# Kernel optimization log

Hardware: AMD Instinct MI355X
Metric: run time of the kernel (lower is better)

The kernel has to match this reference:

```python
import jax, jax.numpy as jnp
import numpy as np

H = 128  # hidden size
I = 256  # input size

def setup_inputs() -> dict:
    key = jax.random.key(0)
    ks = jax.random.split(key, 12)
    s_ih = 1.0 / np.sqrt(H)
    inp = {
        "x": jax.random.normal(ks[0], (256, 512, I), dtype=jnp.float32),
        # PyTorch LSTM params, gate order (i, f, g, o)
        "W_ih": jax.random.uniform(ks[1], (4 * H, I), jnp.float32, -s_ih, s_ih),
        "W_hh": jax.random.uniform(ks[2], (4 * H, H), jnp.float32, -s_ih, s_ih),
        "b_ih": jax.random.uniform(ks[3], (4 * H,), jnp.float32, -s_ih, s_ih),
        "b_hh": jax.random.uniform(ks[4], (4 * H,), jnp.float32, -s_ih, s_ih),
        "W1": jax.random.uniform(ks[5], (64, H), jnp.float32, -1/np.sqrt(H), 1/np.sqrt(H)),
        "b1": jax.random.uniform(ks[6], (64,), jnp.float32, -1/np.sqrt(H), 1/np.sqrt(H)),
        "W2": jax.random.uniform(ks[7], (32, 64), jnp.float32, -1/np.sqrt(64), 1/np.sqrt(64)),
        "b2": jax.random.uniform(ks[8], (32,), jnp.float32, -1/np.sqrt(64), 1/np.sqrt(64)),
        "W3": jax.random.uniform(ks[9], (4, 32), jnp.float32, -1/np.sqrt(32), 1/np.sqrt(32)),
        "b3": jax.random.uniform(ks[10], (4,), jnp.float32, -1/np.sqrt(32), 1/np.sqrt(32)),
    }
    return inp

def _lstm_last_hidden(x, W_ih, W_hh, b_ih, b_hh):
    B = x.shape[0]
    # Precompute input contribution for all timesteps: [B, T, 4H]
    gx = jnp.einsum("bti,gi->btg", x, W_ih) + (b_ih + b_hh)
    gx = jnp.swapaxes(gx, 0, 1)  # [T, B, 4H] for scan over time

    def step(carry, g_x):
        h, c = carry
        gates = g_x + h @ W_hh.T  # [B, 4H]
        i, f, g, o = jnp.split(gates, 4, axis=-1)
        i = jax.nn.sigmoid(i)
        f = jax.nn.sigmoid(f)
        g = jnp.tanh(g)
        o = jax.nn.sigmoid(o)
        c = f * c + i * g
        h = o * jnp.tanh(c)
        return (h, c), None

    h0 = jnp.zeros((B, H), x.dtype)
    (h, _), _ = jax.lax.scan(step, (h0, h0), gx)
    return h  # last-timestep hidden state [B, H]

def reference(x, W_ih, W_hh, b_ih, b_hh, W1, b1, W2, b2, W3, b3):
    h = _lstm_last_hidden(x, W_ih, W_hh, b_ih, b_hh)
    h = jax.nn.relu(h @ W1.T + b1)
    h = jax.nn.relu(h @ W2.T + b2)
    return h @ W3.T + b3  # [B, 4]
```

## Files before the change

kernel.cpp:

```cpp
#include <hip/hip_runtime.h>
#include <hip/hip_bf16.h>


#define TC       64
#define NCHUNK   8
#define BATCH    256
#define TSEQ     512
#define ISZ      256
#define HSZ      128
#define RB       4
#define NBLK     (BATCH / RB)
#define NGB      (2 * TC * 4)
#define HROW     144
#define GX_PER_T 131072
#define GXCH     ((size_t)TC * GX_PER_T)
#define STRT     32768
#define PF       4

#define XN       (BATCH * TSEQ * ISZ)
#define WIHN     (4 * HSZ * ISZ)
#define WHHN     (4 * HSZ * HSZ)
#define CVT_UNITS ((XN + WIHN + WHHN) / 8)

typedef __attribute__((ext_vector_type(8))) short short8;
typedef __attribute__((ext_vector_type(4))) float f32x4;

__device__ __forceinline__ void barrier_nodrain() {
    __asm__ __volatile__("s_waitcnt lgkmcnt(0)\n\ts_barrier" ::: "memory");
}

__device__ __forceinline__ float fast_rcp(float x) {
    return __builtin_amdgcn_rcpf(x);
}
__device__ __forceinline__ float sigmoidf_(float x) {
    return fast_rcp(1.0f + __expf(-x));
}
__device__ __forceinline__ float tanhf_(float x) {
    float e = __expf(2.0f * x);
    return 1.0f - 2.0f * fast_rcp(e + 1.0f);
}
__device__ __forceinline__ unsigned short f2bf(float x) {
    union { float f; unsigned u; } v; v.f = x;
    unsigned r = v.u + 0x7fffu + ((v.u >> 16) & 1u);
    return (unsigned short)(r >> 16);
}
__device__ __forceinline__ float bf2f(unsigned short b) {
    union { unsigned u; float f; } v;
    v.u = ((unsigned)b) << 16;
    return v.f;
}
__device__ __forceinline__ unsigned packbf(float lo, float hi) {
    __hip_bfloat162 h2 = __float22bfloat162_rn(make_float2(lo, hi));
    union { __hip_bfloat162 h; unsigned u; } v; v.h = h2;
    return v.u;
}
__device__ __forceinline__ float sel4(f32x4 v, int r) {
    float s01 = (r & 1) ? v[1] : v[0];
    float s23 = (r & 1) ? v[3] : v[2];
    return (r & 2) ? s23 : s01;
}

__global__ __launch_bounds__(256) void conv_kernel(
    const float* __restrict__ x, const float* __restrict__ Wih,
    const float* __restrict__ Whh,
    unsigned short* __restrict__ xb, unsigned short* __restrict__ wihb,
    unsigned short* __restrict__ whhb)
{
    const size_t stride = (size_t)gridDim.x * 256;
    for (size_t u = (size_t)blockIdx.x * 256 + threadIdx.x; u < (size_t)CVT_UNITS;
         u += stride) {
        const size_t e0 = u * 8;
        const float* s; unsigned short* d;
        if (e0 < (size_t)XN)               { s = x + e0;                 d = xb + e0; }
        else if (e0 < (size_t)(XN + WIHN)) { s = Wih + (e0 - XN);        d = wihb + (e0 - XN); }
        else                               { s = Whh + (e0 - XN - WIHN); d = whhb + (e0 - XN - WIHN); }
        float4 f0 = *(const float4*)(s);
        float4 f1 = *(const float4*)(s + 4);
        *(uint4*)(d) = (uint4){packbf(f0.x, f0.y), packbf(f0.z, f0.w),
                               packbf(f1.x, f1.y), packbf(f1.z, f1.w)};
    }
}

__global__ __launch_bounds__(512, 2) void fused_kernel(
    const unsigned short* __restrict__ xb, const unsigned short* __restrict__ wihb,
    const unsigned short* __restrict__ whhb,
    const float* __restrict__ bih, const float* __restrict__ bhh,
    const unsigned short* __restrict__ gxl, unsigned short* __restrict__ gxg,
    float* __restrict__ hc, int t0, int first, int run_lstm, int run_gemm)
{
    __shared__ __align__(16) char smem[32768];
    const int tid  = threadIdx.x;
    const int w    = tid >> 6;
    const int lane = tid & 63;
    const int n    = lane & 15;
    const int quad = lane >> 4;

    if (blockIdx.x >= NBLK) {
        if (!run_gemm) return;
        short* As = (short*)smem;
        short* Bs = (short*)(smem + 16384);

        const int gb = (int)blockIdx.x - NBLK;
        const int nt = gb & 3;
        const int mt = gb >> 2;
        const int tl = mt >> 1;
        const int b0 = (mt & 1) * 128;
        const int n0 = nt * 128;

        const int mq = w & 1;
        const int nq = w >> 1;

        const int srow = tid >> 2;
        const int skh  = (tid & 3) * 8;

        const unsigned short* xr = xb + ((size_t)(b0 + srow) * TSEQ + (size_t)(t0 + tl)) * ISZ + skh;
        const unsigned short* wr = wihb + (size_t)(n0 + srow) * ISZ + skh;

        f32x4 acc[4][2];
#pragma unroll
        for (int mi = 0; mi < 4; ++mi)
#pragma unroll
            for (int ni = 0; ni < 2; ++ni)
                acc[mi][ni] = (f32x4){0.f, 0.f, 0.f, 0.f};

        *(short8*)(&As[srow * 32 + skh]) = *(const short8*)(xr);
        *(short8*)(&Bs[srow * 32 + skh]) = *(const short8*)(wr);
        barrier_nodrain();

        for (int ks = 0; ks < 8; ++ks) {
            const int cur = (ks & 1) * 4096;
            const int nxt = 4096 - cur;
            short8 va, vb;
            if (ks < 7) {
                va = *(const short8*)(xr + (ks + 1) * 32);
                vb = *(const short8*)(wr + (ks + 1) * 32);
            }
            short8 af[4], bfr[2];
#pragma unroll
            for (int mi = 0; mi < 4; ++mi)
                af[mi] = *(const short8*)(&As[cur + (mq * 64 + mi * 16 + n) * 32 + quad * 8]);
#pragma unroll
            for (int ni = 0; ni < 2; ++ni)
                bfr[ni] = *(const short8*)(&Bs[cur + (nq * 32 + ni * 16 + n) * 32 + quad * 8]);
#pragma unroll
            for (int mi = 0; mi < 4; ++mi)
#pragma unroll
                for (int ni = 0; ni < 2; ++ni)
                    acc[mi][ni] = __builtin_amdgcn_mfma_f32_16x16x32_bf16(
                        af[mi], bfr[ni], acc[mi][ni], 0, 0, 0);
            if (ks < 7) {
                *(short8*)(&As[nxt + srow * 32 + skh]) = va;
                *(short8*)(&Bs[nxt + srow * 32 + skh]) = vb;
            }
            barrier_nodrain();
        }

#pragma unroll
        for (int ni = 0; ni < 2; ++ni) {
            const int j    = nq * 32 + ni * 16 + n;
            const int gate = n0 + j;
            const float bias = bih[gate] + bhh[gate];
            const int wj = nq * 2 + ni;
#pragma unroll
            for (int mi = 0; mi < 4; ++mi) {
                const int bb   = b0 + mq * 64 + mi * 16 + quad * 4;
                const int blk2 = bb >> 2;
                const size_t idx = ((((size_t)nt * TC + tl) * 64 + blk2) * 512) +
                                   (size_t)wj * 64 + (size_t)n * 4;
                const unsigned lo = packbf(acc[mi][ni][0] + bias, acc[mi][ni][1] + bias);
                const unsigned hi = packbf(acc[mi][ni][2] + bias, acc[mi][ni][3] + bias);
                *(uint2*)(&gxg[idx]) = (uint2){lo, hi};
            }
        }
        return;
    }

    if (!run_lstm) return;
    __builtin_amdgcn_s_setprio(1);
    short* h_lds = (short*)smem;

    const int blk  = (int)blockIdx.x;
    const int b0   = blk * RB;
    const int nb   = lane & 3;
    const int jl   = lane >> 2;
    const int j    = 16 * w + jl;
    const int rsel = jl & 3;

    short8 Af[4][4];
#pragma unroll
    for (int g = 0; g < 4; ++g) {
        const unsigned short* rowb = whhb + (size_t)(128 * g + 16 * w + n) * HSZ + 8 * quad;
#pragma unroll
        for (int ks = 0; ks < 4; ++ks)
            Af[g][ks] = *(const short8*)(rowb + 32 * ks);
    }

    float c1 = 0.f, hl1 = 0.f;
    {
        unsigned short h0 = 0;
        if (!first) {
            c1 = hc[(size_t)BATCH * HSZ + (size_t)(b0 + nb) * HSZ + j];
            h0 = f2bf(hc[(size_t)(b0 + nb) * HSZ + j]);
        }
        *(unsigned short*)&h_lds[nb * HROW + j] = h0;
    }

    const unsigned short* gp[4];
#pragma unroll
    for (int g = 0; g < 4; ++g)
        gp[g] = gxl + (((size_t)g * TC) * 64 + blk) * 512 + (size_t)w * 64 + lane;

    unsigned short gq[PF][4];
#pragma unroll
    for (int d = 0; d < PF; ++d)
#pragma unroll
        for (int g = 0; g < 4; ++g)
            gq[d][g] = gp[g][(size_t)d * STRT];

    barrier_nodrain();

    for (int t = 0; t < TC; t += PF) {
#pragma unroll
        for (int u = 0; u < PF; ++u) {
            const int tt = t + u;
            const short* hb_r = h_lds + (u & 1) * (RB * HROW);
            short*       hb_w = h_lds + ((u & 1) ^ 1) * (RB * HROW);

            short8 Bf[4];
#pragma unroll
            for (int ks = 0; ks < 4; ++ks)
                Bf[ks] = *(const short8*)(&hb_r[nb * HROW + 32 * ks + 8 * quad]);

            f32x4 acc[4], acc2[4];
#pragma unroll
            for (int g = 0; g < 4; ++g)
                acc[g] = __builtin_amdgcn_mfma_f32_16x16x32_bf16(
                    Af[g][0], Bf[0], (f32x4){0.f, 0.f, 0.f, 0.f}, 0, 0, 0);
#pragma unroll
            for (int g = 0; g < 4; ++g)
                acc2[g] = __builtin_amdgcn_mfma_f32_16x16x32_bf16(
                    Af[g][1], Bf[1], (f32x4){0.f, 0.f, 0.f, 0.f}, 0, 0, 0);
#pragma unroll
            for (int g = 0; g < 4; ++g)
                acc[g] = __builtin_amdgcn_mfma_f32_16x16x32_bf16(
                    Af[g][2], Bf[2], acc[g], 0, 0, 0);
#pragma unroll
            for (int g = 0; g < 4; ++g)
                acc2[g] = __builtin_amdgcn_mfma_f32_16x16x32_bf16(
                    Af[g][3], Bf[3], acc2[g], 0, 0, 0);
#pragma unroll
            for (int g = 0; g < 4; ++g)
                acc[g] = acc[g] + acc2[g];

            const float s0 = sel4(acc[0], rsel) + bf2f(gq[u][0]);
            const float s1 = sel4(acc[1], rsel) + bf2f(gq[u][1]);
            const float s2 = sel4(acc[2], rsel) + bf2f(gq[u][2]);
            const float s3 = sel4(acc[3], rsel) + bf2f(gq[u][3]);

            const int tf = (tt + PF < TC) ? (tt + PF) : (TC - 1);
#pragma unroll
            for (int g = 0; g < 4; ++g)
                gq[u][g] = gp[g][(size_t)tf * STRT];

            const float ig = sigmoidf_(s0);
            const float fg = sigmoidf_(s1);
            const float gg = tanhf_(s2);
            const float og = sigmoidf_(s3);
            c1  = fg * c1 + ig * gg;
            hl1 = og * tanhf_(c1);

            *(unsigned short*)&hb_w[nb * HROW + j] = f2bf(hl1);
            barrier_nodrain();
        }
    }

    hc[(size_t)(b0 + nb) * HSZ + j] = hl1;
    hc[(size_t)BATCH * HSZ + (size_t)(b0 + nb) * HSZ + j] = c1;
}

__global__ __launch_bounds__(64) void head_kernel(
    const float* __restrict__ hc,
    const float* __restrict__ W1, const float* __restrict__ b1,
    const float* __restrict__ W2, const float* __restrict__ b2,
    const float* __restrict__ W3, const float* __restrict__ b3,
    float* __restrict__ out)
{
    __shared__ float hs[HSZ];
    __shared__ float o1[64];
    __shared__ float o2[32];
    const int bidx = blockIdx.x;
    const int t = threadIdx.x;
    hs[t]      = hc[bidx * HSZ + t];
    hs[t + 64] = hc[bidx * HSZ + t + 64];
    __syncthreads();
    {
        float a = b1[t];
#pragma unroll 8
        for (int k = 0; k < HSZ; ++k) a += W1[t * HSZ + k] * hs[k];
        o1[t] = fmaxf(a, 0.0f);
    }
    __syncthreads();
    if (t < 32) {
        float a = b2[t];
#pragma unroll 8
        for (int k = 0; k < 64; ++k) a += W2[t * 64 + k] * o1[k];
        o2[t] = fmaxf(a, 0.0f);
    }
    __syncthreads();
    if (t < 4) {
        float a = b3[t];
#pragma unroll
        for (int k = 0; k < 32; ++k) a += W3[t * 32 + k] * o2[k];
        out[bidx * 4 + t] = a;
    }
}

extern "C" void kernel_launch(void* const* d_in, const int* in_sizes, int n_in,
                              void* d_out, int out_size, void* d_ws, size_t ws_size,
                              hipStream_t stream) {
    const float* x   = (const float*)d_in[0];
    const float* Wih = (const float*)d_in[1];
    const float* Whh = (const float*)d_in[2];
    const float* bih = (const float*)d_in[3];
    const float* bhh = (const float*)d_in[4];
    const float* W1  = (const float*)d_in[5];
    const float* b1  = (const float*)d_in[6];
    const float* W2  = (const float*)d_in[7];
    const float* b2  = (const float*)d_in[8];
    const float* W3  = (const float*)d_in[9];
    const float* b3  = (const float*)d_in[10];
    float* out = (float*)d_out;

    const size_t GXB = GXCH * sizeof(unsigned short);
    unsigned short* gx0 = (unsigned short*)d_ws;
    unsigned short* gx1 = (unsigned short*)((char*)d_ws + GXB);
    float* hc = (float*)((char*)d_ws + 2 * GXB);
    unsigned short* xb   = (unsigned short*)((char*)d_ws + 2 * GXB + 262144);
    unsigned short* wihb = xb + (size_t)XN;
    unsigned short* whhb = wihb + WIHN;

    conv_kernel<<<dim3(2048), 256, 0, stream>>>(x, Wih, Whh, xb, wihb, whhb);

    for (int k = 0; k <= NCHUNK; ++k) {
        const int run_gemm = (k < NCHUNK);
        const int run_lstm = (k > 0);
        unsigned short* gg = (k & 1) ? gx1 : gx0;
        const unsigned short* gl = ((k - 1) & 1) ? gx1 : gx0;
        fused_kernel<<<dim3(NBLK + NGB), 512, 0, stream>>>(
            xb, wihb, whhb, bih, bhh, gl, gg, hc,
            k * TC, (k == 1) ? 1 : 0, run_lstm, run_gemm);
    }

    head_kernel<<<dim3(BATCH), 64, 0, stream>>>(hc, W1, b1, W2, b2, W3, b3, out);
}
```

Measured before the change: 571.5 us.

## Process 16 batch rows per LSTM block to fill MFMA N dimension

Each recurrent LSTM block now handles 16 batch rows instead of 4, so every lane of the 16x16x32 MFMA output is used and each thread updates four hidden units rather than selecting one. The gate-precompute GEMM writes gx in a new layout that lets each thread load four gate values with one 8-byte read, and h/c state load and store use float4. The number of LSTM blocks drops from 64 to 16, which cuts redundant W_hh register loads and wasted MFMA lanes but serialises four times more activation work per thread on the recurrent critical path. The GEMM epilogue now uses scalar 2-byte stores.

Result: slower. 721.1 us (+26.2%).

```diff
diff --git a/kernel.cpp b/kernel.cpp
--- a/kernel.cpp
+++ b/kernel.cpp
@@ -8,10 +8,10 @@
 #define TSEQ     512
 #define ISZ      256
 #define HSZ      128
-#define RB       4
-#define NBLK     (BATCH / RB)
+#define RB       16
+#define NLB      (BATCH / RB)
 #define NGB      (2 * TC * 4)
-#define HROW     144
+#define HROW     136
 #define GX_PER_T 131072
 #define GXCH     ((size_t)TC * GX_PER_T)
 #define STRT     32768
@@ -44,20 +44,19 @@
     unsigned r = v.u + 0x7fffu + ((v.u >> 16) & 1u);
     return (unsigned short)(r >> 16);
 }
-__device__ __forceinline__ float bf2f(unsigned short b) {
+__device__ __forceinline__ float bfhalf(unsigned wv, int hi) {
     union { unsigned u; float f; } v;
-    v.u = ((unsigned)b) << 16;
+    v.u = hi ? (wv & 0xffff0000u) : (wv << 16);
     return v.f;
+}
+__device__ __forceinline__ float bfh4(uint2 v, int r) {
+    const unsigned wd = (r & 2) ? v.y : v.x;
+    return bfhalf(wd, r & 1);
 }
 __device__ __forceinline__ unsigned packbf(float lo, float hi) {
     __hip_bfloat162 h2 = __float22bfloat162_rn(make_float2(lo, hi));
     union { __hip_bfloat162 h; unsigned u; } v; v.h = h2;
     return v.u;
-}
-__device__ __forceinline__ float sel4(f32x4 v, int r) {
-    float s01 = (r & 1) ? v[1] : v[0];
-    float s23 = (r & 1) ? v[3] : v[2];
-    return (r & 2) ? s23 : s01;
 }
 
 __global__ __launch_bounds__(256) void conv_kernel(
@@ -95,12 +94,12 @@
     const int n    = lane & 15;
     const int quad = lane >> 4;
 
-    if (blockIdx.x >= NBLK) {
+    if (blockIdx.x >= NLB) {
         if (!run_gemm) return;
         short* As = (short*)smem;
         short* Bs = (short*)(smem + 16384);
 
-        const int gb = (int)blockIdx.x - NBLK;
+        const int gb = (int)blockIdx.x - NLB;
         const int nt = gb & 3;
         const int mt = gb >> 2;
         const int tl = mt >> 1;
@@ -160,16 +159,16 @@
             const int j    = nq * 32 + ni * 16 + n;
             const int gate = n0 + j;
             const float bias = bih[gate] + bhh[gate];
-            const int wj = nq * 2 + ni;
+            const int W = nq * 2 + ni;
 #pragma unroll
             for (int mi = 0; mi < 4; ++mi) {
-                const int bb   = b0 + mq * 64 + mi * 16 + quad * 4;
-                const int blk2 = bb >> 2;
-                const size_t idx = ((((size_t)nt * TC + tl) * 64 + blk2) * 512) +
-                                   (size_t)wj * 64 + (size_t)n * 4;
-                const unsigned lo = packbf(acc[mi][ni][0] + bias, acc[mi][ni][1] + bias);
-                const unsigned hi = packbf(acc[mi][ni][2] + bias, acc[mi][ni][3] + bias);
-                *(uint2*)(&gxg[idx]) = (uint2){lo, hi};
+                const int blkp = (b0 >> 4) + mq * 4 + mi;
+                const size_t tb = (((size_t)nt * TC + tl) * 16 + blkp) * 2048 +
+                                  (size_t)W * 256 + (size_t)n;
+#pragma unroll
+                for (int r = 0; r < 4; ++r)
+                    gxg[tb + (size_t)(4 * quad + r) * 16] =
+                        f2bf(acc[mi][ni][r] + bias);
             }
         }
         return;
@@ -179,12 +178,9 @@
     __builtin_amdgcn_s_setprio(1);
     short* h_lds = (short*)smem;
 
-    const int blk  = (int)blockIdx.x;
-    const int b0   = blk * RB;
-    const int nb   = lane & 3;
-    const int jl   = lane >> 2;
-    const int j    = 16 * w + jl;
-    const int rsel = jl & 3;
+    const int blk = (int)blockIdx.x;
+    const int b0  = blk * RB;
+    const int ju  = 16 * w + 4 * quad;
 
     short8 Af[4][4];
 #pragma unroll
@@ -195,27 +191,32 @@
             Af[g][ks] = *(const short8*)(rowb + 32 * ks);
     }
 
-    float c1 = 0.f, hl1 = 0.f;
+    float cst[4], hl[4];
     {
-        unsigned short h0 = 0;
+        uint2 hw = (uint2){0u, 0u};
         if (!first) {
-            c1 = hc[(size_t)BATCH * HSZ + (size_t)(b0 + nb) * HSZ + j];
-            h0 = f2bf(hc[(size_t)(b0 + nb) * HSZ + j]);
+            float4 cv = *(const float4*)(hc + (size_t)BATCH * HSZ + (size_t)(b0 + n) * HSZ + ju);
+            float4 hv = *(const float4*)(hc + (size_t)(b0 + n) * HSZ + ju);
+            cst[0] = cv.x; cst[1] = cv.y; cst[2] = cv.z; cst[3] = cv.w;
+            hw = (uint2){packbf(hv.x, hv.y), packbf(hv.z, hv.w)};
+        } else {
+            cst[0] = cst[1] = cst[2] = cst[3] = 0.f;
         }
-        *(unsigned short*)&h_lds[nb * HROW + j] = h0;
+        hl[0] = hl[1] = hl[2] = hl[3] = 0.f;
+        *(uint2*)(&h_lds[n * HROW + ju]) = hw;
     }
 
     const unsigned short* gp[4];
 #pragma unroll
     for (int g = 0; g < 4; ++g)
-        gp[g] = gxl + (((size_t)g * TC) * 64 + blk) * 512 + (size_t)w * 64 + lane;
-
-    unsigned short gq[PF][4];
+        gp[g] = gxl + ((size_t)g * TC * 16 + blk) * 2048 + w * 256 + n * 16 + 4 * quad;
+
+    uint2 gq[PF][4];
 #pragma unroll
     for (int d = 0; d < PF; ++d)
 #pragma unroll
         for (int g = 0; g < 4; ++g)
-            gq[d][g] = gp[g][(size_t)d * STRT];
+            gq[d][g] = *(const uint2*)(gp[g] + (size_t)d * STRT);
 
     barrier_nodrain();
 
@@ -223,59 +224,58 @@
 #pragma unroll
         for (int u = 0; u < PF; ++u) {
             const int tt = t + u;
-            const short* hb_r = h_lds + (u & 1) * (RB * HROW);
-            short*       hb_w = h_lds + ((u & 1) ^ 1) * (RB * HROW);
+            const short* hb_r = h_lds + (tt & 1) * (RB * HROW);
+            short*       hb_w = h_lds + ((tt & 1) ^ 1) * (RB * HROW);
 
             short8 Bf[4];
 #pragma unroll
             for (int ks = 0; ks < 4; ++ks)
-                Bf[ks] = *(const short8*)(&hb_r[nb * HROW + 32 * ks + 8 * quad]);
-
-            f32x4 acc[4], acc2[4];
+                Bf[ks] = *(const short8*)(&hb_r[n * HROW + 32 * ks + 8 * quad]);
+
+            f32x4 acc[4];
 #pragma unroll
             for (int g = 0; g < 4; ++g)
                 acc[g] = __builtin_amdgcn_mfma_f32_16x16x32_bf16(
                     Af[g][0], Bf[0], (f32x4){0.f, 0.f, 0.f, 0.f}, 0, 0, 0);
 #pragma unroll
+            for (int ks = 1; ks < 4; ++ks)
+#pragma unroll
+                for (int g = 0; g < 4; ++g)
+                    acc[g] = __builtin_amdgcn_mfma_f32_16x16x32_bf16(
+                        Af[g][ks], Bf[ks], acc[g], 0, 0, 0);
+
+            const int tf = (tt + PF < TC) ? (tt + PF) : (TC - 1);
+            uint2 gnew[4];
+#pragma unroll
             for (int g = 0; g < 4; ++g)
-                acc2[g] = __builtin_amdgcn_mfma_f32_16x16x32_bf16(
-                    Af[g][1], Bf[1], (f32x4){0.f, 0.f, 0.f, 0.f}, 0, 0, 0);
-#pragma unroll
-            for (int g = 0; g < 4; ++g)
-                acc[g] = __builtin_amdgcn_mfma_f32_16x16x32_bf16(
-                    Af[g][2], Bf[2], acc[g], 0, 0, 0);
-#pragma unroll
-            for (int g = 0; g < 4; ++g)
-                acc2[g] = __builtin_amdgcn_mfma_f32_16x16x32_bf16(
-                    Af[g][3], Bf[3], acc2[g], 0, 0, 0);
-#pragma unroll
-            for (int g = 0; g < 4; ++g)
-                acc[g] = acc[g] + acc2[g];
-
-            const float s0 = sel4(acc[0], rsel) + bf2f(gq[u][0]);
-            const float s1 = sel4(acc[1], rsel) + bf2f(gq[u][1]);
-            const float s2 = sel4(acc[2], rsel) + bf2f(gq[u][2]);
-            const float s3 = sel4(acc[3], rsel) + bf2f(gq[u][3]);
-
-            const int tf = (tt + PF < TC) ? (tt + PF) : (TC - 1);
-#pragma unroll
-            for (int g = 0; g < 4; ++g)
-                gq[u][g] = gp[g][(size_t)tf * STRT];
-
-            const float ig = sigmoidf_(s0);
-            const float fg = sigmoidf_(s1);
-            const float gg = tanhf_(s2);
-            const float og = sigmoidf_(s3);
-            c1  = fg * c1 + ig * gg;
-            hl1 = og * tanhf_(c1);
-
-            *(unsigned short*)&hb_w[nb * HROW + j] = f2bf(hl1);
+                gnew[g] = *(const uint2*)(gp[g] + (size_t)tf * STRT);
+
+#pragma unroll
+            for (int r = 0; r < 4; ++r) {
+                const float s0 = acc[0][r] + bfh4(gq[u][0], r);
+                const float s1 = acc[1][r] + bfh4(gq[u][1], r);
+                const float s2 = acc[2][r] + bfh4(gq[u][2], r);
+                const float s3 = acc[3][r] + bfh4(gq[u][3], r);
+                const float ig = sigmoidf_(s0);
+                const float fg = sigmoidf_(s1);
+                const float gg = tanhf_(s2);
+                const float og = sigmoidf_(s3);
+                cst[r] = fg * cst[r] + ig * gg;
+                hl[r]  = og * tanhf_(cst[r]);
+            }
+#pragma unroll
+            for (int g = 0; g < 4; ++g) gq[u][g] = gnew[g];
+
+            *(uint2*)(&hb_w[n * HROW + ju]) =
+                (uint2){packbf(hl[0], hl[1]), packbf(hl[2], hl[3])};
             barrier_nodrain();
         }
     }
 
-    hc[(size_t)(b0 + nb) * HSZ + j] = hl1;
-    hc[(size_t)BATCH * HSZ + (size_t)(b0 + nb) * HSZ + j] = c1;
+    *(float4*)(&hc[(size_t)(b0 + n) * HSZ + ju]) =
+        (float4){hl[0], hl[1], hl[2], hl[3]};
+    *(float4*)(&hc[(size_t)BATCH * HSZ + (size_t)(b0 + n) * HSZ + ju]) =
+        (float4){cst[0], cst[1], cst[2], cst[3]};
 }
 
 __global__ __launch_bounds__(64) void head_kernel(
@@ -346,7 +346,7 @@
         const int run_lstm = (k > 0);
         unsigned short* gg = (k & 1) ? gx1 : gx0;
         const unsigned short* gl = ((k - 1) & 1) ? gx1 : gx0;
-        fused_kernel<<<dim3(NBLK + NGB), 512, 0, stream>>>(
+        fused_kernel<<<dim3(NLB + NGB), 512, 0, stream>>>(
             xb, wihb, whhb, bih, bhh, gl, gg, hc,
             k * TC, (k == 1) ? 1 : 0, run_lstm, run_gemm);
     }
```
